# Kernel tuning notes

Hardware: AMD Instinct MI355X
Metric: run time of the kernel (lower is better)

Reference implementation:

```python
import jax, jax.numpy as jnp
import numpy as np
import math

T = 2048
D_MODEL = 2048
N_H = 16
D_H = D_MODEL // N_H
EPS = 1e-5


def _rope_tables(t, d_h):
    # standard RoPE cos/sin tables, full head-dim layout matching rotate_half
    inv_freq = 1.0 / (10000.0 ** (jnp.arange(0, d_h // 2, dtype=jnp.float32) / (d_h // 2)))
    ang = jnp.arange(t, dtype=jnp.float32)[:, None] * inv_freq[None, :]  # (T, d_h/2)
    ang = jnp.concatenate([ang, ang], axis=-1)  # (T, d_h)
    return jnp.cos(ang), jnp.sin(ang)


def setup_inputs() -> dict:
    key = jax.random.key(0)
    kx, kq, kk, kv, ko = jax.random.split(key, 5)
    scale = 1.0 / math.sqrt(D_MODEL)
    cos, sin = _rope_tables(T, D_H)
    return {
        "x": jax.random.normal(kx, (T, D_MODEL), dtype=jnp.float32),
        "cos": cos,
        "sin": sin,
        "attention_mask": jnp.ones((T,), dtype=jnp.int32),
        "ln_w": jnp.ones((D_MODEL,), dtype=jnp.float32),
        "Wq": jax.random.normal(kq, (D_MODEL, D_MODEL), dtype=jnp.float32) * scale,
        "Wk": jax.random.normal(kk, (D_MODEL, D_MODEL), dtype=jnp.float32) * scale,
        "Wv": jax.random.normal(kv, (D_MODEL, D_MODEL), dtype=jnp.float32) * scale,
        "Wo": jax.random.normal(ko, (D_MODEL, D_MODEL), dtype=jnp.float32) * scale,
    }


def _rotate_half(x):
    x1, x2 = jnp.split(x, 2, axis=-1)
    return jnp.concatenate((-x2, x1), axis=-1)


def reference(x, cos, sin, attention_mask, ln_w, Wq, Wk, Wv, Wo):
    t = x.shape[0]
    # RMSNorm
    var = jnp.mean(x * x, axis=-1, keepdims=True)
    h = ln_w * x * jax.lax.rsqrt(var + EPS)
    # QKV projections (eqx Linear: weight @ x => x @ W.T), reshape to (n_h, T, d_h)
    q = (h @ Wq.T).reshape(t, N_H, D_H).transpose(1, 0, 2)
    k = (h @ Wk.T).reshape(t, N_H, D_H).transpose(1, 0, 2)
    v = (h @ Wv.T).reshape(t, N_H, D_H).transpose(1, 0, 2)
    # RoPE (cos/sin broadcast (T,d_h) -> (n_h,T,d_h))
    q = q * cos + _rotate_half(q) * sin
    k = k * cos + _rotate_half(k) * sin
    scores = jnp.einsum('hqd,hkd->hqk', q, k) / math.sqrt(D_H)
    causal = jnp.tril(jnp.ones((t, t), dtype=bool))[None]
    neg = jnp.finfo(scores.dtype).min
    am = attention_mask.astype(bool)
    allowed = causal & am[None, None, :]
    scores = jnp.where(allowed, scores, neg)
    scores = jnp.where(am[None, :, None], scores, neg)
    probs = jax.nn.softmax(scores, axis=-1)
    out = jnp.einsum('hqk,hkd->hqd', probs, v).transpose(1, 0, 2).reshape(t, -1)
    out = out @ Wo.T
    out = jnp.where(am[:, None], out, 0.0)
    return x + out
```

## Files before the change

### kernel.cpp

```cpp
#include <hip/hip_runtime.h>
#include <stdint.h>

#define TS 2048
#define DM 2048
#define NH 16
#define DH 128

typedef unsigned short u16t;
typedef __attribute__((ext_vector_type(8))) short short8;
typedef __attribute__((ext_vector_type(4))) float f32x4;
typedef __attribute__((ext_vector_type(4))) unsigned int u32x4;
typedef __attribute__((ext_vector_type(4))) unsigned short u16x4;

__device__ __forceinline__ float bf2f(u16t b) {
  return __uint_as_float(((unsigned int)b) << 16);
}
__device__ __forceinline__ u16t f2bf(float f) {
  unsigned int u = __float_as_uint(f);
  u += 0x7FFFu + ((u >> 16) & 1u);
  return (u16t)(u >> 16);
}

__device__ __forceinline__ void async_copy16(const u16t* g, u16t* l) {
  __builtin_amdgcn_global_load_lds((const __attribute__((address_space(1))) void*)g,
                                   (__attribute__((address_space(3))) void*)l, 16, 0, 0);
}

#define DPP_ROR_F(x, n) __uint_as_float(__builtin_amdgcn_update_dpp( \
    0, (int)__float_as_uint(x), 0x120 | (n), 0xF, 0xF, true))

__device__ __forceinline__ float row16_max(float x) {
  x = fmaxf(x, DPP_ROR_F(x, 8));
  x = fmaxf(x, DPP_ROR_F(x, 4));
  x = fmaxf(x, DPP_ROR_F(x, 2));
  x = fmaxf(x, DPP_ROR_F(x, 1));
  return x;
}
__device__ __forceinline__ float row16_sum(float x) {
  x += DPP_ROR_F(x, 8);
  x += DPP_ROR_F(x, 4);
  x += DPP_ROR_F(x, 2);
  x += DPP_ROR_F(x, 1);
  return x;
}

__global__ __launch_bounds__(256) void cast_rms_kernel(const float* __restrict__ W0,
                                                       const float* __restrict__ W1,
                                                       const float* __restrict__ W2,
                                                       const float* __restrict__ W3,
                                                       u16t* __restrict__ outw,
                                                       const float* __restrict__ x,
                                                       const float* __restrict__ lnw,
                                                       u16t* __restrict__ h) {
  if (blockIdx.x < 16384) {
    const int idx = blockIdx.x * 256 + threadIdx.x;
    const int mat = idx >> 20;
    const size_t off = (size_t)(idx & 0xFFFFF) * 4;
    const float* W = (mat == 0) ? W0 : (mat == 1) ? W1 : (mat == 2) ? W2 : W3;
    const f32x4 v = *(const f32x4*)(W + off);
    size_t dstoff = off;
    if (mat < 2) {
      const int row = (int)(off >> 11);
      const int col = (int)(off & 2047);
      const int d = row & 127;
      const int e = d & 63;
      const int p = ((e >> 4) * 32 + (e & 15)) + ((d >> 6) << 4);
      dstoff = ((size_t)((row & ~127) | p) << 11) | (size_t)col;
    }
    union { u16t s[4]; uint64_t u; } o;
#pragma unroll
    for (int i = 0; i < 4; ++i) o.s[i] = f2bf(v[i]);
    *(uint64_t*)(outw + (size_t)mat * (DM * DM) + dstoff) = o.u;
    return;
  }
  const int row = blockIdx.x - 16384;
  const int tid = threadIdx.x;
  const float* xr = x + (size_t)row * DM + tid * 8;
  f32x4 v0 = *(const f32x4*)(xr);
  f32x4 v1 = *(const f32x4*)(xr + 4);
  float f[8];
#pragma unroll
  for (int i = 0; i < 4; ++i) { f[i] = v0[i]; f[i + 4] = v1[i]; }
  float ss = 0.f;
#pragma unroll
  for (int i = 0; i < 8; ++i) ss += f[i] * f[i];
#pragma unroll
  for (int off = 1; off < 64; off <<= 1) ss += __shfl_xor(ss, off, 64);
  __shared__ float wsum[4];
  if ((tid & 63) == 0) wsum[tid >> 6] = ss;
  __syncthreads();
  float tot = wsum[0] + wsum[1] + wsum[2] + wsum[3];
  float rs = rsqrtf(tot * (1.0f / DM) + 1e-5f);
  f32x4 w0 = *(const f32x4*)(lnw + tid * 8);
  f32x4 w1 = *(const f32x4*)(lnw + tid * 8 + 4);
  u32x4 o;
#pragma unroll
  for (int i = 0; i < 4; ++i) {
    unsigned int lo = f2bf(f[2 * i]     * ((2 * i     < 4) ? w0[2 * i]     : w1[2 * i - 4]) * rs);
    unsigned int hi = f2bf(f[2 * i + 1] * ((2 * i + 1 < 4) ? w0[2 * i + 1] : w1[2 * i - 3]) * rs);
    o[i] = lo | (hi << 16);
  }
  *(u32x4*)(h + (size_t)row * DM + tid * 8) = o;
}

__global__ __launch_bounds__(512, 2) void gemm_qkv(
    const u16t* __restrict__ A,
    const u16t* __restrict__ B0, const u16t* __restrict__ B1, const u16t* __restrict__ B2,
    u16t* __restrict__ Cq, u16t* __restrict__ Ck, u16t* __restrict__ Cv,
    const float* __restrict__ cosb, const float* __restrict__ sinb) {
  __shared__ u16t Ab[2][128 * 64];
  __shared__ u16t Bb[3][2][128 * 64];
  const int tid  = threadIdx.x;
  const int wave = tid >> 6;
  const int lane = tid & 63;
  const int quad = lane >> 4;
  const int c16  = lane & 15;
  const int h7   = c16 & 7;
  const int wm   = wave >> 2;
  const int wn   = wave & 3;
  const int bid  = blockIdx.x;
  const int wgid = (bid & 7) * 32 + (bid >> 3);
  const int m0   = (wgid & 15) * 128;
  const int n0   = (wgid >> 4) * 128;

  const int srow = lane >> 3;
  const int sg   = (lane & 7) ^ srow;
  auto stage = [&](int d, int k0) {
    const size_t koff = (size_t)k0 + sg * 8;
#pragma unroll
    for (int c = 0; c < 2; ++c) {
      const int rb = wave * 16 + c * 8;
      async_copy16(A  + (size_t)(m0 + rb + srow) * DM + koff, &Ab[d][rb * 64]);
      async_copy16(B0 + (size_t)(n0 + rb + srow) * DM + koff, &Bb[0][d][rb * 64]);
      async_copy16(B1 + (size_t)(n0 + rb + srow) * DM + koff, &Bb[1][d][rb * 64]);
      async_copy16(B2 + (size_t)(n0 + rb + srow) * DM + koff, &Bb[2][d][rb * 64]);
    }
  };

  const f32x4 fzero = {0.f, 0.f, 0.f, 0.f};
  f32x4 acc[3][4][2];
#pragma unroll
  for (int m = 0; m < 3; ++m)
#pragma unroll
    for (int i = 0; i < 4; ++i)
#pragma unroll
      for (int j = 0; j < 2; ++j) acc[m][i][j] = fzero;

  stage(0, 0);
  asm volatile("s_waitcnt vmcnt(0)" ::: "memory");
  __builtin_amdgcn_s_barrier();

  for (int kt = 0; kt < DM / 64; ++kt) {
    const int cur = kt & 1;
    if (kt + 1 < DM / 64) stage(cur ^ 1, (kt + 1) * 64);
    const u16t* Abuf = Ab[cur];
    __builtin_amdgcn_s_setprio(1);
#pragma unroll
    for (int ks = 0; ks < 2; ++ks) {
      const int gsw = ((ks * 4 + quad) ^ h7) * 8;
      short8 af[4], bfr[3][2];
#pragma unroll
      for (int i = 0; i < 4; ++i)
        af[i] = *(const short8*)(Abuf + (wm * 64 + i * 16 + c16) * 64 + gsw);
#pragma unroll
      for (int m = 0; m < 3; ++m)
#pragma unroll
        for (int nt = 0; nt < 2; ++nt)
          bfr[m][nt] = *(const short8*)(&Bb[m][cur][0] + (wn * 32 + nt * 16 + c16) * 64 + gsw);
#pragma unroll
      for (int m = 0; m < 3; ++m)
#pragma unroll
        for (int i = 0; i < 4; ++i)
#pragma unroll
          for (int nt = 0; nt < 2; ++nt)
            acc[m][i][nt] =
                __builtin_amdgcn_mfma_f32_16x16x32_bf16(af[i], bfr[m][nt], acc[m][i][nt], 0, 0, 0);
    }
    __builtin_amdgcn_s_setprio(0);
    asm volatile("s_waitcnt vmcnt(0)" ::: "memory");
    __builtin_amdgcn_s_barrier();
  }

#pragma unroll
  for (int mat = 0; mat < 2; ++mat) {
    u16t* C = mat ? Ck : Cq;
#pragma unroll
    for (int mt = 0; mt < 4; ++mt) {
#pragma unroll
      for (int r = 0; r < 4; ++r) {
        const int row = m0 + wm * 64 + mt * 16 + quad * 4 + r;
        const size_t base = (size_t)row * DM;
        const int col = n0 + wn * 32 + c16;
        const int p = col & 127;
        const int dorig = ((p >> 5) << 4) + c16;
        const float cv = cosb[row * DH + dorig];
        const float sv = sinb[row * DH + dorig];
        const float x1 = acc[mat][mt][0][r];
        const float x2 = acc[mat][mt][1][r];
        C[base + col]      = f2bf(x1 * cv - x2 * sv);
        C[base + col + 16] = f2bf(x2 * cv + x1 * sv);
      }
    }
  }
#pragma unroll
  for (int mt = 0; mt < 4; ++mt) {
#pragma unroll
    for (int r = 0; r < 4; ++r) {
      const int row = m0 + wm * 64 + mt * 16 + quad * 4 + r;
#pragma unroll
      for (int nt = 0; nt < 2; ++nt) {
        const int col = n0 + wn * 32 + nt * 16 + c16;
        Cv[(size_t)col * TS + row] = f2bf(acc[2][mt][nt][r]);
      }
    }
  }
}

__global__ __launch_bounds__(512, 2) void gemm_out(
    const u16t* __restrict__ A, const u16t* __restrict__ B0,
    u16t* __restrict__ P0, u16t* __restrict__ P1,
    u16t* __restrict__ P2, u16t* __restrict__ P3) {
  __shared__ u16t Ab[2][256 * 64];
  __shared__ u16t Bb[2][256 * 64];
  const int tid  = threadIdx.x;
  const int wave = tid >> 6;
  const int lane = tid & 63;
  const int quad = lane >> 4;
  const int c16  = lane & 15;
  const int h7   = c16 & 7;
  const int wm   = wave >> 2;
  const int wn   = wave & 3;
  const int nwg  = gridDim.x;
  const int bid  = blockIdx.x;
  const int wgid = (bid & 7) * (nwg >> 3) + (bid >> 3);
  const int mat  = wgid >> 6;
  const int rem  = wgid & 63;
  const int m0   = (rem & 7) * 256;
  const int n0   = ((rem >> 3) & 7) * 256;
  const int kbeg = mat * (DM / 4);
  const int NT   = DM / 4 / 64;

  const int srow = lane >> 3;
  const int sg   = (lane & 7) ^ srow;
  auto stage = [&](int d, int k0) {
    const size_t koff = (size_t)k0 + sg * 8;
#pragma unroll
    for (int c = 0; c < 4; ++c) {
      const int rb = wave * 32 + c * 8;
      async_copy16(A + (size_t)(m0 + rb + srow) * DM + koff, &Ab[d][rb * 64]);
      async_copy16(B0 + (size_t)(n0 + rb + srow) * DM + koff, &Bb[d][rb * 64]);
    }
  };

  const f32x4 fzero = {0.f, 0.f, 0.f, 0.f};
  f32x4 acc[8][4];
#pragma unroll
  for (int i = 0; i < 8; ++i)
#pragma unroll
    for (int j = 0; j < 4; ++j) acc[i][j] = fzero;

  stage(0, kbeg);
  asm volatile("s_waitcnt vmcnt(0)" ::: "memory");
  __builtin_amdgcn_s_barrier();

  for (int kt = 0; kt < NT; ++kt) {
    const int cur = kt & 1;
    if (kt + 1 < NT) stage(cur ^ 1, kbeg + (kt + 1) * 64);
    const u16t* Abuf = Ab[cur];
    const u16t* Bbuf = Bb[cur];
    __builtin_amdgcn_s_setprio(1);
#pragma unroll
    for (int ks = 0; ks < 2; ++ks) {
      short8 af[8], bfr[4];
#pragma unroll
      for (int i = 0; i < 8; ++i) {
        const int row = wm * 128 + i * 16 + c16;
        af[i] = *(const short8*)(Abuf + row * 64 + (((ks * 4 + quad) ^ h7) * 8));
      }
#pragma unroll
      for (int nt = 0; nt < 4; ++nt) {
        const int row = wn * 64 + nt * 16 + c16;
        bfr[nt] = *(const short8*)(Bbuf + row * 64 + (((ks * 4 + quad) ^ h7) * 8));
      }
#pragma unroll
      for (int i = 0; i < 8; ++i)
#pragma unroll
        for (int nt = 0; nt < 4; ++nt)
          acc[i][nt] =
              __builtin_amdgcn_mfma_f32_16x16x32_bf16(af[i], bfr[nt], acc[i][nt], 0, 0, 0);
    }
    __builtin_amdgcn_s_setprio(0);
    asm volatile("s_waitcnt vmcnt(0)" ::: "memory");
    __builtin_amdgcn_s_barrier();
  }

  u16t* P = (mat == 0) ? P0 : (mat == 1) ? P1 : (mat == 2) ? P2 : P3;
#pragma unroll
  for (int mt = 0; mt < 8; ++mt) {
#pragma unroll
    for (int r = 0; r < 4; ++r) {
      const int row = m0 + wm * 128 + mt * 16 + quad * 4 + r;
      const size_t base = (size_t)row * DM;
#pragma unroll
      for (int nt = 0; nt < 4; ++nt) {
        const int col = n0 + wn * 64 + nt * 16 + c16;
        P[base + col] = f2bf(acc[mt][nt][r]);
      }
    }
  }
}

__global__ __launch_bounds__(256) void combine4_kernel(const u16t* __restrict__ P0,
                                                       const u16t* __restrict__ P1,
                                                       const u16t* __restrict__ P2,
                                                       const u16t* __restrict__ P3,
                                                       const float* __restrict__ x,
                                                       const int* __restrict__ am,
                                                       float* __restrict__ out) {
  const size_t idx = ((size_t)blockIdx.x * 256 + threadIdx.x) * 4;
  const int row = (int)(idx >> 11);
  const float mk = (am[row] != 0) ? 1.f : 0.f;
  const u16x4 a = *(const u16x4*)(P0 + idx);
  const u16x4 b = *(const u16x4*)(P1 + idx);
  const u16x4 c = *(const u16x4*)(P2 + idx);
  const u16x4 d = *(const u16x4*)(P3 + idx);
  const f32x4 xr = *(const f32x4*)(x + idx);
  f32x4 o;
#pragma unroll
  for (int i = 0; i < 4; ++i)
    o[i] = xr[i] + mk * ((bf2f(a[i]) + bf2f(b[i])) + (bf2f(c[i]) + bf2f(d[i])));
  *(f32x4*)(out + idx) = o;
}

__global__ __launch_bounds__(256) void attn_kernel(const u16t* __restrict__ Q,
                                                   const u16t* __restrict__ K,
                                                   const u16t* __restrict__ Vt,
                                                   const int* __restrict__ am,
                                                   u16t* __restrict__ O) {
  __shared__ u16t Klds[128 * 128];
  __shared__ u16t Vlds[128 * 128];
  __shared__ u16t Plds[4][2048];
  const int wave = threadIdx.x >> 6;
  const int lane = threadIdx.x & 63;
  const int x    = blockIdx.x;
  const int half = x >> 8;
  const int idx  = x & 255;
  const int head = idx & (NH - 1);
  const int grp  = idx >> 4;
  const int qt   = half ? grp : (TS / 64 - 1 - grp);
  const int q0   = qt * 64 + wave * 16;
  const int quad = lane >> 4;
  const int c16  = lane & 15;
  const u16t* Qh  = Q + head * DH;
  const u16t* Kh  = K + head * DH;
  const u16t* Vth = Vt + (size_t)head * DH * TS;
  u16t* Pw = Plds[wave];

  const int row_s = (lane >> 4);
  const int g_s   = (lane & 15);

  short8 qf[4];
#pragma unroll
  for (int dc = 0; dc < 4; ++dc)
    qf[dc] = *(const short8*)(Qh + (size_t)(q0 + c16) * DM + dc * 32 + quad * 8);

  const f32x4 fzero = {0.f, 0.f, 0.f, 0.f};
  float m_run[4], l_run[4];
  f32x4 o_acc[8];
#pragma unroll
  for (int r = 0; r < 4; ++r) { m_run[r] = -1e30f; l_run[r] = 0.f; }
#pragma unroll
  for (int nt = 0; nt < 8; ++nt) o_acc[nt] = fzero;

  const float scale = 0.08838834764831845f;
  const int ntiles = (qt * 64 + 191) >> 7;

  for (int kt = 0; kt < ntiles; ++kt) {
    const int k0 = kt * 128;
    __syncthreads();
#pragma unroll
    for (int c = 0; c < 8; ++c) {
      const int ch = wave * 8 + c;
      const int r  = 4 * ch + row_s;
      const int g  = g_s ^ (r & 15);
      async_copy16(Kh + (size_t)(k0 + r) * DM + g * 8, Klds + ch * 512);
      async_copy16(Vth + (size_t)r * TS + k0 + g * 8, Vlds + ch * 512);
    }
    __syncthreads();

    f32x4 s[8];
#pragma unroll
    for (int ns = 0; ns < 8; ++ns) {
      f32x4 sa = fzero;
      const int rr = ns * 16 + c16;
#pragma unroll
      for (int dc = 0; dc < 4; ++dc) {
        short8 kf = *(const short8*)(Klds + rr * 128 + (((dc * 4 + quad) ^ c16) * 8));
        sa = __builtin_amdgcn_mfma_f32_16x16x32_bf16(qf[dc], kf, sa, 0, 0, 0);
      }
      s[ns] = sa;
    }

    float pv[8][4], tmax[4];
#pragma unroll
    for (int r = 0; r < 4; ++r) tmax[r] = -1e30f;
#pragma unroll
    for (int ns = 0; ns < 8; ++ns) {
      const int key = k0 + ns * 16 + c16;
      const bool kok = (am[key] != 0);
#pragma unroll
      for (int r = 0; r < 4; ++r) {
        const int qrow = q0 + quad * 4 + r;
        float v = s[ns][r] * scale;
        if (key > qrow || !kok) v = -1e30f;
        pv[ns][r] = v;
        tmax[r] = fmaxf(tmax[r], v);
      }
    }
    float alpha[4], rsum[4];
#pragma unroll
    for (int r = 0; r < 4; ++r) {
      const float mn = fmaxf(m_run[r], row16_max(tmax[r]));
      alpha[r] = __expf(m_run[r] - mn);
      m_run[r] = mn;
      float rs = 0.f;
#pragma unroll
      for (int ns = 0; ns < 8; ++ns) {
        const float e = __expf(pv[ns][r] - mn);
        pv[ns][r] = e;
        rs += e;
      }
      rsum[r] = row16_sum(rs);
      l_run[r] = l_run[r] * alpha[r] + rsum[r];
    }

#pragma unroll
    for (int ns = 0; ns < 8; ++ns)
#pragma unroll
      for (int r = 0; r < 4; ++r)
        Pw[(ns >> 1) * 512 + (quad * 4 + r) * 32 + (ns & 1) * 16 + c16] = f2bf(pv[ns][r]);
    asm volatile("s_waitcnt lgkmcnt(0)" ::: "memory");
    short8 pf[4];
#pragma unroll
    for (int c = 0; c < 4; ++c)
      pf[c] = *(const short8*)(Pw + c * 512 + c16 * 32 + quad * 8);

#pragma unroll
    for (int nt = 0; nt < 8; ++nt)
#pragma unroll
      for (int r = 0; r < 4; ++r) o_acc[nt][r] *= alpha[r];
#pragma unroll
    for (int nt = 0; nt < 8; ++nt) {
      const int rr = nt * 16 + c16;
#pragma unroll
      for (int c = 0; c < 4; ++c) {
        short8 vf = *(const short8*)(Vlds + rr * 128 + (((c * 4 + quad) ^ c16) * 8));
        o_acc[nt] = __builtin_amdgcn_mfma_f32_16x16x32_bf16(pf[c], vf, o_acc[nt], 0, 0, 0);
      }
    }
  }

#pragma unroll
  for (int r = 0; r < 4; ++r) {
    const float inv = 1.0f / fmaxf(l_run[r], 1e-20f);
    const int qrow = q0 + quad * 4 + r;
#pragma unroll
    for (int nt = 0; nt < 8; ++nt)
      O[(size_t)qrow * DM + head * DH + nt * 16 + c16] = f2bf(o_acc[nt][r] * inv);
  }
}

extern "C" void kernel_launch(void* const* d_in, const int* in_sizes, int n_in,
                              void* d_out, int out_size, void* d_ws, size_t ws_size,
                              hipStream_t stream) {
  const float* x    = (const float*)d_in[0];
  const float* cosb = (const float*)d_in[1];
  const float* sinb = (const float*)d_in[2];
  const int*   am   = (const int*)d_in[3];
  const float* lnw  = (const float*)d_in[4];
  const float* Wq   = (const float*)d_in[5];
  const float* Wk   = (const float*)d_in[6];
  const float* Wv   = (const float*)d_in[7];
  const float* Wo   = (const float*)d_in[8];
  float* out = (float*)d_out;

  u16t* h    = (u16t*)d_ws;
  u16t* Q    = h + (size_t)TS * DM;
  u16t* K    = Q + (size_t)TS * DM;
  u16t* Vt   = K + (size_t)TS * DM;
  u16t* attn = Vt + (size_t)TS * DM;
  u16t* Wb   = attn + (size_t)TS * DM;
  u16t* Wqb = Wb;
  u16t* Wkb = Wb + (size_t)DM * DM;
  u16t* Wvb = Wb + 2 * (size_t)DM * DM;
  u16t* Wob = Wb + 3 * (size_t)DM * DM;

  cast_rms_kernel<<<16384 + TS, 256, 0, stream>>>(Wq, Wk, Wv, Wo, Wb, x, lnw, h);
  gemm_qkv<<<256, 512, 0, stream>>>(h, Wqb, Wkb, Wvb, Q, K, Vt, cosb, sinb);
  attn_kernel<<<NH * (TS / 64), 256, 0, stream>>>(Q, K, Vt, am, attn);
  gemm_out<<<256, 512, 0, stream>>>(attn, Wob, h, Q, K, Vt);
  combine4_kernel<<<(TS * DM / 4) / 256, 256, 0, stream>>>(h, Q, K, Vt, x, am, out);
}
```

Measured before the change: 281.3 us.

## Double-buffer K/V tiles with 64-key blocks in attention kernel

Shrinks the attention key tile from 128 to 64 keys and double-buffers the K and V LDS tiles, so the async global-to-LDS load of the next tile overlaps compute on the current one. The tighter causal bound (qt+1 tiles of 64) removes some fully masked key work on diagonal blocks. It also adds XOR swizzles to the P scratch buffer to reduce LDS bank conflicts. The cost is more loop iterations with their own barriers and softmax rescale steps, and a smaller MFMA batch per iteration.

```diff
diff --git a/kernel.cpp b/kernel.cpp
--- a/kernel.cpp
+++ b/kernel.cpp
@@ -337,9 +337,9 @@
                                                    const u16t* __restrict__ Vt,
                                                    const int* __restrict__ am,
                                                    u16t* __restrict__ O) {
-  __shared__ u16t Klds[128 * 128];
-  __shared__ u16t Vlds[128 * 128];
-  __shared__ u16t Plds[4][2048];
+  __shared__ u16t Klds[2][64 * 128];
+  __shared__ u16t Vlds[2][128 * 64];
+  __shared__ u16t Plds[4][1024];
   const int wave = threadIdx.x >> 6;
   const int lane = threadIdx.x & 63;
   const int x    = blockIdx.x;
@@ -356,8 +356,22 @@
   const u16t* Vth = Vt + (size_t)head * DH * TS;
   u16t* Pw = Plds[wave];
 
-  const int row_s = (lane >> 4);
-  const int g_s   = (lane & 15);
+  const int krow = lane >> 4;
+  const int kg_s = lane & 15;
+  const int vrow = lane >> 3;
+  const int vg_s = (lane & 7) ^ vrow;
+
+  auto stageKV = [&](int d, int k0) {
+#pragma unroll
+    for (int c = 0; c < 4; ++c) {
+      const int ch = wave * 4 + c;
+      const int kr = 4 * ch + krow;
+      async_copy16(Kh + (size_t)(k0 + kr) * DM + ((kg_s ^ (kr & 15)) * 8),
+                   Klds[d] + ch * 512);
+      const int vr = 8 * ch + vrow;
+      async_copy16(Vth + (size_t)vr * TS + k0 + vg_s * 8, Vlds[d] + ch * 512);
+    }
+  };
 
   short8 qf[4];
 #pragma unroll
@@ -373,39 +387,35 @@
   for (int nt = 0; nt < 8; ++nt) o_acc[nt] = fzero;
 
   const float scale = 0.08838834764831845f;
-  const int ntiles = (qt * 64 + 191) >> 7;
+  const int ntiles = qt + 1;
+
+  stageKV(0, 0);
+  asm volatile("s_waitcnt vmcnt(0)" ::: "memory");
+  __builtin_amdgcn_s_barrier();
 
   for (int kt = 0; kt < ntiles; ++kt) {
-    const int k0 = kt * 128;
-    __syncthreads();
-#pragma unroll
-    for (int c = 0; c < 8; ++c) {
-      const int ch = wave * 8 + c;
-      const int r  = 4 * ch + row_s;
-      const int g  = g_s ^ (r & 15);
-      async_copy16(Kh + (size_t)(k0 + r) * DM + g * 8, Klds + ch * 512);
-      async_copy16(Vth + (size_t)r * TS + k0 + g * 8, Vlds + ch * 512);
-    }
-    __syncthreads();
-
-    f32x4 s[8];
-#pragma unroll
-    for (int ns = 0; ns < 8; ++ns) {
+    const int cur = kt & 1;
+    const int k0 = kt * 64;
+    if (kt + 1 < ntiles) stageKV(cur ^ 1, k0 + 64);
+
+    f32x4 s[4];
+#pragma unroll
+    for (int ns = 0; ns < 4; ++ns) {
       f32x4 sa = fzero;
       const int rr = ns * 16 + c16;
 #pragma unroll
       for (int dc = 0; dc < 4; ++dc) {
-        short8 kf = *(const short8*)(Klds + rr * 128 + (((dc * 4 + quad) ^ c16) * 8));
+        short8 kf = *(const short8*)(Klds[cur] + rr * 128 + (((dc * 4 + quad) ^ c16) * 8));
         sa = __builtin_amdgcn_mfma_f32_16x16x32_bf16(qf[dc], kf, sa, 0, 0, 0);
       }
       s[ns] = sa;
     }
 
-    float pv[8][4], tmax[4];
+    float pv[4][4], tmax[4];
 #pragma unroll
     for (int r = 0; r < 4; ++r) tmax[r] = -1e30f;
 #pragma unroll
-    for (int ns = 0; ns < 8; ++ns) {
+    for (int ns = 0; ns < 4; ++ns) {
       const int key = k0 + ns * 16 + c16;
       const bool kok = (am[key] != 0);
 #pragma unroll
@@ -417,7 +427,7 @@
         tmax[r] = fmaxf(tmax[r], v);
       }
     }
-    float alpha[4], rsum[4];
+    float alpha[4];
 #pragma unroll
     for (int r = 0; r < 4; ++r) {
       const float mn = fmaxf(m_run[r], row16_max(tmax[r]));
@@ -425,25 +435,25 @@
       m_run[r] = mn;
       float rs = 0.f;
 #pragma unroll
-      for (int ns = 0; ns < 8; ++ns) {
+      for (int ns = 0; ns < 4; ++ns) {
         const float e = __expf(pv[ns][r] - mn);
         pv[ns][r] = e;
         rs += e;
       }
-      rsum[r] = row16_sum(rs);
-      l_run[r] = l_run[r] * alpha[r] + rsum[r];
-    }
-
-#pragma unroll
-    for (int ns = 0; ns < 8; ++ns)
+      l_run[r] = l_run[r] * alpha[r] + row16_sum(rs);
+    }
+
+#pragma unroll
+    for (int ns = 0; ns < 4; ++ns)
 #pragma unroll
       for (int r = 0; r < 4; ++r)
-        Pw[(ns >> 1) * 512 + (quad * 4 + r) * 32 + (ns & 1) * 16 + c16] = f2bf(pv[ns][r]);
+        Pw[(ns >> 1) * 512 + (quad * 4 + r) * 32 +
+           ((((ns & 1) * 2 + (c16 >> 3)) ^ quad) & 3) * 8 + (c16 & 7)] = f2bf(pv[ns][r]);
     asm volatile("s_waitcnt lgkmcnt(0)" ::: "memory");
-    short8 pf[4];
-#pragma unroll
-    for (int c = 0; c < 4; ++c)
-      pf[c] = *(const short8*)(Pw + c * 512 + c16 * 32 + quad * 8);
+    short8 pf[2];
+#pragma unroll
+    for (int c = 0; c < 2; ++c)
+      pf[c] = *(const short8*)(Pw + c * 512 + c16 * 32 + ((quad ^ (c16 >> 2)) & 3) * 8);
 
 #pragma unroll
     for (int nt = 0; nt < 8; ++nt)
@@ -453,11 +463,14 @@
     for (int nt = 0; nt < 8; ++nt) {
       const int rr = nt * 16 + c16;
 #pragma unroll
-      for (int c = 0; c < 4; ++c) {
-        short8 vf = *(const short8*)(Vlds + rr * 128 + (((c * 4 + quad) ^ c16) * 8));
+      for (int c = 0; c < 2; ++c) {
+        short8 vf = *(const short8*)(Vlds[cur] + rr * 64 + (((c * 4 + quad) ^ (c16 & 7)) * 8));
         o_acc[nt] = __builtin_amdgcn_mfma_f32_16x16x32_bf16(pf[c], vf, o_acc[nt], 0, 0, 0);
       }
     }
+
+    asm volatile("s_waitcnt vmcnt(0)" ::: "memory");
+    __builtin_amdgcn_s_barrier();
   }
 
 #pragma unroll
```

Measured after the change: 299.1 us. 6.3% more time.

## Replace split-K output GEMM with 128x128 tiles and fused residual epilogue

Applied to the files above, without the earlier changes.

The output projection previously split K four ways over 256x256 tiles, wrote four bf16 partial products, and ran a separate combine kernel that summed them with the residual and mask. It now uses 128x128 tiles over the full K range with 256 workgroups and writes x + mask*acc directly in fp32. This removes the partial-product traffic, the extra bf16 rounding and one kernel launch. In exchange, per-tile arithmetic intensity is lower and each workgroup runs a longer serial K loop.

```diff
diff --git a/kernel.cpp b/kernel.cpp
--- a/kernel.cpp
+++ b/kernel.cpp
@@ -218,10 +218,10 @@
 
 __global__ __launch_bounds__(512, 2) void gemm_out(
     const u16t* __restrict__ A, const u16t* __restrict__ B0,
-    u16t* __restrict__ P0, u16t* __restrict__ P1,
-    u16t* __restrict__ P2, u16t* __restrict__ P3) {
-  __shared__ u16t Ab[2][256 * 64];
-  __shared__ u16t Bb[2][256 * 64];
+    const float* __restrict__ xres, const int* __restrict__ am,
+    float* __restrict__ out) {
+  __shared__ u16t Ab[2][128 * 64];
+  __shared__ u16t Bb[2][128 * 64];
   const int tid  = threadIdx.x;
   const int wave = tid >> 6;
   const int lane = tid & 63;
@@ -230,62 +230,54 @@
   const int h7   = c16 & 7;
   const int wm   = wave >> 2;
   const int wn   = wave & 3;
-  const int nwg  = gridDim.x;
   const int bid  = blockIdx.x;
-  const int wgid = (bid & 7) * (nwg >> 3) + (bid >> 3);
-  const int mat  = wgid >> 6;
-  const int rem  = wgid & 63;
-  const int m0   = (rem & 7) * 256;
-  const int n0   = ((rem >> 3) & 7) * 256;
-  const int kbeg = mat * (DM / 4);
-  const int NT   = DM / 4 / 64;
+  const int wgid = (bid & 7) * 32 + (bid >> 3);
+  const int m0   = (wgid & 15) * 128;
+  const int n0   = (wgid >> 4) * 128;
 
   const int srow = lane >> 3;
   const int sg   = (lane & 7) ^ srow;
   auto stage = [&](int d, int k0) {
     const size_t koff = (size_t)k0 + sg * 8;
 #pragma unroll
-    for (int c = 0; c < 4; ++c) {
-      const int rb = wave * 32 + c * 8;
-      async_copy16(A + (size_t)(m0 + rb + srow) * DM + koff, &Ab[d][rb * 64]);
+    for (int c = 0; c < 2; ++c) {
+      const int rb = wave * 16 + c * 8;
+      async_copy16(A  + (size_t)(m0 + rb + srow) * DM + koff, &Ab[d][rb * 64]);
       async_copy16(B0 + (size_t)(n0 + rb + srow) * DM + koff, &Bb[d][rb * 64]);
     }
   };
 
   const f32x4 fzero = {0.f, 0.f, 0.f, 0.f};
-  f32x4 acc[8][4];
-#pragma unroll
-  for (int i = 0; i < 8; ++i)
-#pragma unroll
-    for (int j = 0; j < 4; ++j) acc[i][j] = fzero;
-
-  stage(0, kbeg);
+  f32x4 acc[4][2];
+#pragma unroll
+  for (int i = 0; i < 4; ++i)
+#pragma unroll
+    for (int j = 0; j < 2; ++j) acc[i][j] = fzero;
+
+  stage(0, 0);
   asm volatile("s_waitcnt vmcnt(0)" ::: "memory");
   __builtin_amdgcn_s_barrier();
 
-  for (int kt = 0; kt < NT; ++kt) {
+  for (int kt = 0; kt < DM / 64; ++kt) {
     const int cur = kt & 1;
-    if (kt + 1 < NT) stage(cur ^ 1, kbeg + (kt + 1) * 64);
+    if (kt + 1 < DM / 64) stage(cur ^ 1, (kt + 1) * 64);
     const u16t* Abuf = Ab[cur];
     const u16t* Bbuf = Bb[cur];
     __builtin_amdgcn_s_setprio(1);
 #pragma unroll
     for (int ks = 0; ks < 2; ++ks) {
-      short8 af[8], bfr[4];
-#pragma unroll
-      for (int i = 0; i < 8; ++i) {
-        const int row = wm * 128 + i * 16 + c16;
-        af[i] = *(const short8*)(Abuf + row * 64 + (((ks * 4 + quad) ^ h7) * 8));
-      }
-#pragma unroll
-      for (int nt = 0; nt < 4; ++nt) {
-        const int row = wn * 64 + nt * 16 + c16;
-        bfr[nt] = *(const short8*)(Bbuf + row * 64 + (((ks * 4 + quad) ^ h7) * 8));
-      }
-#pragma unroll
-      for (int i = 0; i < 8; ++i)
-#pragma unroll
-        for (int nt = 0; nt < 4; ++nt)
+      const int gsw = ((ks * 4 + quad) ^ h7) * 8;
+      short8 af[4], bfr[2];
+#pragma unroll
+      for (int i = 0; i < 4; ++i)
+        af[i] = *(const short8*)(Abuf + (wm * 64 + i * 16 + c16) * 64 + gsw);
+#pragma unroll
+      for (int nt = 0; nt < 2; ++nt)
+        bfr[nt] = *(const short8*)(Bbuf + (wn * 32 + nt * 16 + c16) * 64 + gsw);
+#pragma unroll
+      for (int i = 0; i < 4; ++i)
+#pragma unroll
+        for (int nt = 0; nt < 2; ++nt)
           acc[i][nt] =
               __builtin_amdgcn_mfma_f32_16x16x32_bf16(af[i], bfr[nt], acc[i][nt], 0, 0, 0);
     }
@@ -294,42 +286,20 @@
     __builtin_amdgcn_s_barrier();
   }
 
-  u16t* P = (mat == 0) ? P0 : (mat == 1) ? P1 : (mat == 2) ? P2 : P3;
-#pragma unroll
-  for (int mt = 0; mt < 8; ++mt) {
+#pragma unroll
+  for (int mt = 0; mt < 4; ++mt) {
 #pragma unroll
     for (int r = 0; r < 4; ++r) {
-      const int row = m0 + wm * 128 + mt * 16 + quad * 4 + r;
+      const int row = m0 + wm * 64 + mt * 16 + quad * 4 + r;
+      const float mk = (am[row] != 0) ? 1.f : 0.f;
       const size_t base = (size_t)row * DM;
 #pragma unroll
-      for (int nt = 0; nt < 4; ++nt) {
-        const int col = n0 + wn * 64 + nt * 16 + c16;
-        P[base + col] = f2bf(acc[mt][nt][r]);
-      }
-    }
-  }
-}
-
-__global__ __launch_bounds__(256) void combine4_kernel(const u16t* __restrict__ P0,
-                                                       const u16t* __restrict__ P1,
-                                                       const u16t* __restrict__ P2,
-                                                       const u16t* __restrict__ P3,
-                                                       const float* __restrict__ x,
-                                                       const int* __restrict__ am,
-                                                       float* __restrict__ out) {
-  const size_t idx = ((size_t)blockIdx.x * 256 + threadIdx.x) * 4;
-  const int row = (int)(idx >> 11);
-  const float mk = (am[row] != 0) ? 1.f : 0.f;
-  const u16x4 a = *(const u16x4*)(P0 + idx);
-  const u16x4 b = *(const u16x4*)(P1 + idx);
-  const u16x4 c = *(const u16x4*)(P2 + idx);
-  const u16x4 d = *(const u16x4*)(P3 + idx);
-  const f32x4 xr = *(const f32x4*)(x + idx);
-  f32x4 o;
-#pragma unroll
-  for (int i = 0; i < 4; ++i)
-    o[i] = xr[i] + mk * ((bf2f(a[i]) + bf2f(b[i])) + (bf2f(c[i]) + bf2f(d[i])));
-  *(f32x4*)(out + idx) = o;
+      for (int nt = 0; nt < 2; ++nt) {
+        const int col = n0 + wn * 32 + nt * 16 + c16;
+        out[base + col] = xres[base + col] + mk * acc[mt][nt][r];
+      }
+    }
+  }
 }
 
 __global__ __launch_bounds__(256) void attn_kernel(const u16t* __restrict__ Q,
@@ -498,6 +468,5 @@
   cast_rms_kernel<<<16384 + TS, 256, 0, stream>>>(Wq, Wk, Wv, Wo, Wb, x, lnw, h);
   gemm_qkv<<<256, 512, 0, stream>>>(h, Wqb, Wkb, Wvb, Q, K, Vt, cosb, sinb);
   attn_kernel<<<NH * (TS / 64), 256, 0, stream>>>(Q, K, Vt, am, attn);
-  gemm_out<<<256, 512, 0, stream>>>(attn, Wob, h, Q, K, Vt);
-  combine4_kernel<<<(TS * DM / 4) / 256, 256, 0, stream>>>(h, Q, K, Vt, x, am, out);
-}
+  gemm_out<<<256, 512, 0, stream>>>(attn, Wob, x, am, out);
+}
```

Measured after the change: 283.5 us. Within noise of the previous version (+0.8%).
